# Kernel optimization log

Measured on AMD Instinct MI355X. Metric: run time of the kernel, lower is better.

The kernel has to match this reference:

```python
import jax, jax.numpy as jnp
import numpy as np

H, W = 8, 8
N = 1 + H * W          # 65 tokens (cls + patches)
DIM = 128
HEADS = 8
DH = 32
INNER = HEADS * DH     # 256
B = 64
EPS = 1e-5


def setup_inputs() -> dict:
    key = jax.random.key(0)
    ks = jax.random.split(key, 7)
    x = jax.random.normal(ks[0], (B, N, DIM), dtype=jnp.float32)
    gamma = jnp.ones((DIM,), jnp.float32)
    beta = jnp.zeros((DIM,), jnp.float32)
    # kaiming_uniform-ish init scale for linear weights
    s_qk = float(np.sqrt(1.0 / DIM))
    Wqk = jax.random.uniform(ks[1], (DIM, 2 * INNER), jnp.float32, -s_qk, s_qk)
    # per-(query, key)-position value weights: [n, n, dim, inner]
    Wv = jax.random.uniform(ks[2], (N, N, DIM, INNER), jnp.float32, -s_qk, s_qk)
    s_o = float(np.sqrt(1.0 / INNER))
    Wout = jax.random.uniform(ks[3], (INNER, DIM), jnp.float32, -s_o, s_o)
    bout = jax.random.uniform(ks[4], (DIM,), jnp.float32, -s_o, s_o)
    return {"x": x, "gamma": gamma, "beta": beta, "Wqk": Wqk, "Wv": Wv,
            "Wout": Wout, "bout": bout}


def reference(x, gamma, beta, Wqk, Wv, Wout, bout):
    b, n, d = x.shape
    # LayerNorm
    mu = jnp.mean(x, axis=-1, keepdims=True)
    var = jnp.mean(jnp.square(x - mu), axis=-1, keepdims=True)
    xn = (x - mu) / jnp.sqrt(var + EPS) * gamma + beta
    # q, k projections
    qk = xn @ Wqk                               # [b, n, 2*inner]
    q, k = jnp.split(qk, 2, axis=-1)
    q = q.reshape(b, n, HEADS, DH).transpose(0, 2, 1, 3)  # [b, h, n, dh]
    k = k.reshape(b, n, HEADS, DH).transpose(0, 2, 1, 3)
    scale = DH ** -0.5
    dots = jnp.einsum('bhnd,bhmd->bhnm', q, k) * scale
    attn = jax.nn.softmax(dots, axis=-1)        # [b, h, n, m]
    # per-(n,m) value: v[b,n,m] = xn[b,n] @ Wv[n,m]  -> [b, n, m, inner]
    v = jnp.einsum('bnd,nmde->bnme', xn, Wv)
    v = v.reshape(b, n, n, HEADS, DH)           # [b, n, m, h, dh]
    # weighted sum over keys m
    out = jnp.einsum('bhnm,bnmhd->bnhd', attn, v).reshape(b, n, INNER)
    return out @ Wout + bout
```

## Files before the change

kernel.cpp:

```cpp
#include <hip/hip_runtime.h>

#define EPS 1e-5f

typedef __attribute__((ext_vector_type(8))) short short8;
typedef __attribute__((ext_vector_type(4))) float float4v;

__device__ __forceinline__ unsigned short f2bf(float x) {
  unsigned int u = __builtin_bit_cast(unsigned int, x);
  u += 0x7fffu + ((u >> 16) & 1u);
  return (unsigned short)(u >> 16);
}
__device__ __forceinline__ float bf2f(unsigned short h) {
  unsigned int u = ((unsigned int)h) << 16;
  return __builtin_bit_cast(float, u);
}

__global__ __launch_bounds__(256) void ln_kernel(
    const float* __restrict__ x, const float* __restrict__ gamma,
    const float* __restrict__ beta, float* __restrict__ xn,
    float* __restrict__ inner) {
  {
    const int zi = blockIdx.x * 1024 + threadIdx.x * 4;
    float4 z; z.x = 0.f; z.y = 0.f; z.z = 0.f; z.w = 0.f;
    *(float4*)(inner + zi) = z;
  }
  const int row = blockIdx.x * 4 + (threadIdx.x >> 6);
  const int lane = threadIdx.x & 63;
  const float2 v = ((const float2*)(x + (size_t)row * 128))[lane];
  float s = v.x + v.y;
#pragma unroll
  for (int off = 1; off < 64; off <<= 1) s += __shfl_xor(s, off);
  const float mu = s * (1.f / 128.f);
  const float dx = v.x - mu, dy = v.y - mu;
  float qv = dx * dx + dy * dy;
#pragma unroll
  for (int off = 1; off < 64; off <<= 1) qv += __shfl_xor(qv, off);
  const float rstd = 1.f / sqrtf(qv * (1.f / 128.f) + EPS);
  const float2 g = ((const float2*)gamma)[lane];
  const float2 be = ((const float2*)beta)[lane];
  float2 o;
  o.x = dx * rstd * g.x + be.x;
  o.y = dy * rstd * g.y + be.y;
  ((float2*)(xn + (size_t)row * 128))[lane] = o;
}

__global__ __launch_bounds__(256) void qk_kernel(
    const float* __restrict__ xn, const float* __restrict__ Wqk,
    float* __restrict__ qk) {
  __shared__ float xsx[32][130];
  __shared__ float wsx[128][68];
  const int t = threadIdx.x;
  const int r0 = blockIdx.x * 32, c0 = blockIdx.y * 64;
  for (int i = t; i < 32 * 32; i += 256) {
    int r = i >> 5, c = (i & 31) << 2;
    float4 v = *(const float4*)(xn + (size_t)(r0 + r) * 128 + c);
    float* dst = &xsx[r][c];
    dst[0] = v.x; dst[1] = v.y; dst[2] = v.z; dst[3] = v.w;
  }
  for (int i = t; i < 128 * 16; i += 256) {
    int k = i >> 4, c = (i & 15) << 2;
    *(float4*)&wsx[k][c] = *(const float4*)(Wqk + (size_t)k * 512 + c0 + c);
  }
  __syncthreads();
  const int rr = (t >> 4) * 2, cc = (t & 15) * 4;
  float acc[2][4] = {{0.f, 0.f, 0.f, 0.f}, {0.f, 0.f, 0.f, 0.f}};
  for (int k = 0; k < 128; k++) {
    float4 wv4 = *(const float4*)&wsx[k][cc];
    float x0 = xsx[rr][k], x1 = xsx[rr + 1][k];
    acc[0][0] += x0 * wv4.x; acc[0][1] += x0 * wv4.y;
    acc[0][2] += x0 * wv4.z; acc[0][3] += x0 * wv4.w;
    acc[1][0] += x1 * wv4.x; acc[1][1] += x1 * wv4.y;
    acc[1][2] += x1 * wv4.z; acc[1][3] += x1 * wv4.w;
  }
#pragma unroll
  for (int r = 0; r < 2; r++) {
    float4 o;
    o.x = acc[r][0]; o.y = acc[r][1]; o.z = acc[r][2]; o.w = acc[r][3];
    *(float4*)(qk + (size_t)(r0 + rr + r) * 512 + c0 + cc) = o;
  }
}

__global__ __launch_bounds__(256) void softmax_kernel(
    const float* __restrict__ qk, float* __restrict__ attn) {
  const int b = blockIdx.x >> 3, h = blockIdx.x & 7;
  __shared__ float qs[65][33];
  __shared__ float ks[65][33];
  __shared__ float dotsS[65][66];
  __shared__ float rsum[65];
  const int t = threadIdx.x;
  for (int i = t; i < 65 * 32; i += 256) {
    int n = i >> 5, d = i & 31;
    size_t base = ((size_t)b * 65 + n) * 512 + h * 32 + d;
    qs[n][d] = qk[base];
    ks[n][d] = qk[base + 256];
  }
  __syncthreads();
  const float scale = 0.17677669529663687f;
  for (int i = t; i < 65 * 65; i += 256) {
    int n = i / 65, mm = i - n * 65;
    float s = 0.f;
#pragma unroll
    for (int d = 0; d < 32; d++) s += qs[n][d] * ks[mm][d];
    dotsS[n][mm] = s * scale;
  }
  __syncthreads();
  if (t < 65) {
    float mx = -1e30f;
    for (int mm = 0; mm < 65; mm++) mx = fmaxf(mx, dotsS[t][mm]);
    float sum = 0.f;
    for (int mm = 0; mm < 65; mm++) {
      float e = __expf(dotsS[t][mm] - mx);
      dotsS[t][mm] = e;
      sum += e;
    }
    rsum[t] = 1.f / sum;
  }
  __syncthreads();
  const size_t obase = ((size_t)b * 8 + h) * 65 * 65;
  for (int i = t; i < 65 * 65; i += 256) {
    int n = i / 65;
    attn[obase + i] = dotsS[n][i - n * 65] * rsum[n];
  }
}

__global__ __launch_bounds__(512, 2) void attnv_kernel(
    const float* __restrict__ xn, const float* __restrict__ attn,
    const float* __restrict__ Wv, float* __restrict__ inner) {
  __shared__ __align__(16) char sbuf[131072];
  __shared__ float attnL[5 * 8 * 64];
  float* xs = (float*)sbuf;
  unsigned short* wvb = (unsigned short*)sbuf;

  const int nq = blockIdx.x;
  const int mc = blockIdx.y;
  const int ms = (mc * 65) >> 4;
  const int cnt = (((mc + 1) * 65) >> 4) - ms;

  const int t = threadIdx.x;
  const int lane = t & 63;
  const int w = t >> 6;
  const int er = lane & 15, q = lane >> 4;
  const int rg = w & 1, cg = w >> 1;

  const int eS = t & 255;
  const int dS0 = (t >> 8) << 6;
  const float* wq = Wv + ((size_t)nq * 65 + ms) * 32768 + (size_t)dS0 * 256 + eS;

  float stg[64];

#define ISSUE(mm) do {                                                        \
    const float* p_ = wq + (size_t)(mm) * 32768;                              \
    _Pragma("unroll")                                                         \
    for (int i_ = 0; i_ < 64; i_++)                                           \
      stg[i_] = __builtin_nontemporal_load(p_ + (size_t)i_ * 256);            \
  } while (0)

#define CONVWRITE(buf) do {                                                   \
    unsigned short* wb_ = wvb + (size_t)(buf) * 32768 + eS * 128;             \
    const int cb_ = (t >> 8) << 3;                                            \
    _Pragma("unroll")                                                         \
    for (int jj_ = 0; jj_ < 8; jj_++) {                                       \
      short8 pk_;                                                             \
      _Pragma("unroll")                                                       \
      for (int j_ = 0; j_ < 8; j_++) pk_[j_] = (short)f2bf(stg[jj_ * 8 + j_]);\
      *(short8*)&wb_[((cb_ + jj_) ^ (eS & 15)) << 3] = pk_;                   \
    }                                                                         \
  } while (0)

  ISSUE(0);

  const int tot = cnt << 9;
  for (int i = t; i < tot; i += 512) {
    int mloc = i % cnt;
    int rest = i / cnt;
    int h = rest & 7;
    int b = rest >> 3;
    attnL[(mloc * 8 + h) * 64 + b] =
        attn[(((size_t)(b * 8 + h) * 65) + nq) * 65 + ms + mloc];
  }
  for (int i = t; i < 64 * 32; i += 512) {
    int b = i >> 5, c = (i & 31) << 2;
    float4 v = *(const float4*)(xn + ((size_t)b * 65 + nq) * 128 + c);
    float* dst = xs + b * 130 + c;
    dst[0] = v.x; dst[1] = v.y; dst[2] = v.z; dst[3] = v.w;
  }
  __syncthreads();

  short8 ah[2][4], al[2][4];
#pragma unroll
  for (int rt = 0; rt < 2; rt++) {
    const int arow = rg * 32 + rt * 16 + er;
#pragma unroll
    for (int s = 0; s < 4; s++) {
#pragma unroll
      for (int j = 0; j < 8; j++) {
        float xv = xs[arow * 130 + s * 32 + q * 8 + j];
        unsigned short hi = f2bf(xv);
        ah[rt][s][j] = (short)hi;
        al[rt][s][j] = (short)f2bf(xv - bf2f(hi));
      }
    }
  }
  __syncthreads();

  CONVWRITE(0);
  __syncthreads();

  float4v acc[2][4];
#pragma unroll
  for (int rt = 0; rt < 2; rt++)
#pragma unroll
    for (int ct = 0; ct < 4; ct++)
      acc[rt][ct] = (float4v){0.f, 0.f, 0.f, 0.f};

  for (int i = 0; i < cnt; i++) {
    if (i + 1 < cnt) ISSUE(i + 1);
    const unsigned short* wb = wvb + (size_t)(i & 1) * 32768;
    float4v P[2][4];
#pragma unroll
    for (int rt = 0; rt < 2; rt++)
#pragma unroll
      for (int ct = 0; ct < 4; ct++)
        P[rt][ct] = (float4v){0.f, 0.f, 0.f, 0.f};
    __builtin_amdgcn_s_setprio(1);
#pragma unroll
    for (int s = 0; s < 4; s++) {
      const int kc = 4 * s + q;
#pragma unroll
      for (int ct = 0; ct < 4; ct++) {
        short8 bf = *(const short8*)&wb[(cg * 64 + ct * 16 + er) * 128 + ((kc ^ er) << 3)];
        P[0][ct] = __builtin_amdgcn_mfma_f32_16x16x32_bf16(ah[0][s], bf, P[0][ct], 0, 0, 0);
        P[0][ct] = __builtin_amdgcn_mfma_f32_16x16x32_bf16(al[0][s], bf, P[0][ct], 0, 0, 0);
        P[1][ct] = __builtin_amdgcn_mfma_f32_16x16x32_bf16(ah[1][s], bf, P[1][ct], 0, 0, 0);
        P[1][ct] = __builtin_amdgcn_mfma_f32_16x16x32_bf16(al[1][s], bf, P[1][ct], 0, 0, 0);
      }
    }
    __builtin_amdgcn_s_setprio(0);
#pragma unroll
    for (int rt = 0; rt < 2; rt++) {
#pragma unroll
      for (int ct = 0; ct < 4; ct++) {
        const int h = cg * 2 + (ct >> 1);
        const float* ap = attnL + (i * 8 + h) * 64 + rg * 32 + rt * 16 + q * 4;
#pragma unroll
        for (int r = 0; r < 4; r++) acc[rt][ct][r] += ap[r] * P[rt][ct][r];
      }
    }
    if (i + 1 < cnt) CONVWRITE((i + 1) & 1);
    __syncthreads();
  }

#undef ISSUE
#undef CONVWRITE

#pragma unroll
  for (int rt = 0; rt < 2; rt++) {
#pragma unroll
    for (int ct = 0; ct < 4; ct++) {
      const int ecol = cg * 64 + ct * 16 + er;
#pragma unroll
      for (int r = 0; r < 4; r++) {
        const int b = rg * 32 + rt * 16 + q * 4 + r;
        atomicAdd(inner + ((size_t)b * 65 + nq) * 256 + ecol, acc[rt][ct][r]);
      }
    }
  }
}

__global__ __launch_bounds__(256) void outproj_kernel(
    const float* __restrict__ inner, const float* __restrict__ Wout,
    const float* __restrict__ bout, float* __restrict__ out) {
  __shared__ float isx[16][258];
  __shared__ float wsx[64][132];
  const int t = threadIdx.x;
  const int r0 = blockIdx.x * 16;
  for (int i = t; i < 16 * 64; i += 256) {
    int r = i >> 6, c = (i & 63) << 2;
    float4 v = *(const float4*)(inner + (size_t)(r0 + r) * 256 + c);
    float* dst = &isx[r][c];
    dst[0] = v.x; dst[1] = v.y; dst[2] = v.z; dst[3] = v.w;
  }
  const int rr = (t >> 5) * 2, cc = (t & 31) * 4;
  float acc[2][4] = {{0.f, 0.f, 0.f, 0.f}, {0.f, 0.f, 0.f, 0.f}};
  for (int kc = 0; kc < 4; kc++) {
    __syncthreads();
    for (int i = t; i < 64 * 32; i += 256) {
      int k = i >> 5, c = (i & 31) << 2;
      *(float4*)&wsx[k][c] = *(const float4*)(Wout + (size_t)(kc * 64 + k) * 128 + c);
    }
    __syncthreads();
#pragma unroll 8
    for (int k = 0; k < 64; k++) {
      float4 wv4 = *(const float4*)&wsx[k][cc];
      float x0 = isx[rr][kc * 64 + k];
      float x1 = isx[rr + 1][kc * 64 + k];
      acc[0][0] += x0 * wv4.x; acc[0][1] += x0 * wv4.y;
      acc[0][2] += x0 * wv4.z; acc[0][3] += x0 * wv4.w;
      acc[1][0] += x1 * wv4.x; acc[1][1] += x1 * wv4.y;
      acc[1][2] += x1 * wv4.z; acc[1][3] += x1 * wv4.w;
    }
  }
  float4 bb = *(const float4*)(bout + cc);
#pragma unroll
  for (int r = 0; r < 2; r++) {
    float4 o;
    o.x = acc[r][0] + bb.x; o.y = acc[r][1] + bb.y;
    o.z = acc[r][2] + bb.z; o.w = acc[r][3] + bb.w;
    *(float4*)(out + (size_t)(r0 + rr + r) * 128 + cc) = o;
  }
}

extern "C" void kernel_launch(void* const* d_in, const int* in_sizes, int n_in,
                              void* d_out, int out_size, void* d_ws, size_t ws_size,
                              hipStream_t stream) {
  const float* x     = (const float*)d_in[0];
  const float* gamma = (const float*)d_in[1];
  const float* beta  = (const float*)d_in[2];
  const float* Wqk   = (const float*)d_in[3];
  const float* Wv    = (const float*)d_in[4];
  const float* Wout  = (const float*)d_in[5];
  const float* bout  = (const float*)d_in[6];
  float* out = (float*)d_out;
  float* ws  = (float*)d_ws;

  float* xn    = ws;
  float* qk    = ws + 532480;
  float* attn  = ws + 2662400;
  float* inner = ws + 4825600;

  ln_kernel<<<1040, 256, 0, stream>>>(x, gamma, beta, xn, inner);
  qk_kernel<<<dim3(130, 8), 256, 0, stream>>>(xn, Wqk, qk);
  softmax_kernel<<<512, 256, 0, stream>>>(qk, attn);
  attnv_kernel<<<dim3(65, 16), 512, 0, stream>>>(xn, attn, Wv, inner);
  outproj_kernel<<<260, 256, 0, stream>>>(inner, Wout, bout, out);
}
```

Measured before the change: 806.0 us.

## Pre-convert Wv to swizzled bf16, stream it via global_load_lds, drop atomics

A new conv_kernel converts the fp32 Wv to bf16 once per call. It writes it into workspace already XOR-swizzled to match the LDS layout. attnv then copies tiles straight into LDS with global_load_lds instead of doing per-thread fp32 loads plus conversion, and the grid is reshaped: 256 threads, half the output columns per block, 8 key chunks. The atomicAdd into inner is replaced by per-chunk partial buffers that outproj sums, which also removes the zeroing in ln_kernel. The trade-off is that total DRAM traffic on Wv grows, since it is read as fp32, written as bf16 and read again, in exchange for a simpler, more latency-tolerant inner loop.

```diff
diff --git a/kernel.cpp b/kernel.cpp
--- a/kernel.cpp
+++ b/kernel.cpp
@@ -15,15 +15,39 @@
   return __builtin_bit_cast(float, u);
 }
 
+__device__ __forceinline__ void gl_lds16(const void* g, void* l) {
+  __builtin_amdgcn_global_load_lds(
+      (const __attribute__((address_space(1))) unsigned int*)g,
+      (__attribute__((address_space(3))) unsigned int*)l, 16, 0, 0);
+}
+
+__global__ __launch_bounds__(256) void conv_kernel(
+    const float* __restrict__ Wv, unsigned short* __restrict__ Wvb) {
+  const int blk = blockIdx.x;
+  const int t = threadIdx.x;
+  const float* src = Wv + (size_t)blk * 32768 + t;
+  char* dst = (char*)Wvb + (size_t)blk * 65536 + t * 256;
+  const int x = t & 15;
+#pragma unroll
+  for (int p = 0; p < 8; p++) {
+    float v[16];
+#pragma unroll
+    for (int j = 0; j < 16; j++)
+      v[j] = __builtin_nontemporal_load(src + (size_t)(p * 16 + j) * 256);
+    short8 a, b;
+#pragma unroll
+    for (int j = 0; j < 8; j++) {
+      a[j] = (short)f2bf(v[j]);
+      b[j] = (short)f2bf(v[8 + j]);
+    }
+    *(short8*)(dst + (((2 * p) ^ x) << 4)) = a;
+    *(short8*)(dst + (((2 * p + 1) ^ x) << 4)) = b;
+  }
+}
+
 __global__ __launch_bounds__(256) void ln_kernel(
     const float* __restrict__ x, const float* __restrict__ gamma,
-    const float* __restrict__ beta, float* __restrict__ xn,
-    float* __restrict__ inner) {
-  {
-    const int zi = blockIdx.x * 1024 + threadIdx.x * 4;
-    float4 z; z.x = 0.f; z.y = 0.f; z.z = 0.f; z.w = 0.f;
-    *(float4*)(inner + zi) = z;
-  }
+    const float* __restrict__ beta, float* __restrict__ xn) {
   const int row = blockIdx.x * 4 + (threadIdx.x >> 6);
   const int lane = threadIdx.x & 63;
   const float2 v = ((const float2*)(x + (size_t)row * 128))[lane];
@@ -123,69 +147,35 @@
   }
 }
 
-__global__ __launch_bounds__(512, 2) void attnv_kernel(
+__global__ __launch_bounds__(256, 2) void attnv_kernel(
     const float* __restrict__ xn, const float* __restrict__ attn,
-    const float* __restrict__ Wv, float* __restrict__ inner) {
-  __shared__ __align__(16) char sbuf[131072];
-  __shared__ float attnL[5 * 8 * 64];
+    const unsigned short* __restrict__ Wvb, float* __restrict__ inner_p) {
+  __shared__ __align__(16) char sbuf[65536];
+  __shared__ float attnL[9 * 4 * 64];
   float* xs = (float*)sbuf;
   unsigned short* wvb = (unsigned short*)sbuf;
 
-  const int nq = blockIdx.x;
+  const int nq = blockIdx.x >> 1, eh = blockIdx.x & 1;
   const int mc = blockIdx.y;
-  const int ms = (mc * 65) >> 4;
-  const int cnt = (((mc + 1) * 65) >> 4) - ms;
+  const int ms = (mc * 65) >> 3;
+  const int cnt = (((mc + 1) * 65) >> 3) - ms;
 
   const int t = threadIdx.x;
   const int lane = t & 63;
   const int w = t >> 6;
   const int er = lane & 15, q = lane >> 4;
   const int rg = w & 1, cg = w >> 1;
-
-  const int eS = t & 255;
-  const int dS0 = (t >> 8) << 6;
-  const float* wq = Wv + ((size_t)nq * 65 + ms) * 32768 + (size_t)dS0 * 256 + eS;
-
-  float stg[64];
-
-#define ISSUE(mm) do {                                                        \
-    const float* p_ = wq + (size_t)(mm) * 32768;                              \
-    _Pragma("unroll")                                                         \
-    for (int i_ = 0; i_ < 64; i_++)                                           \
-      stg[i_] = __builtin_nontemporal_load(p_ + (size_t)i_ * 256);            \
-  } while (0)
-
-#define CONVWRITE(buf) do {                                                   \
-    unsigned short* wb_ = wvb + (size_t)(buf) * 32768 + eS * 128;             \
-    const int cb_ = (t >> 8) << 3;                                            \
-    _Pragma("unroll")                                                         \
-    for (int jj_ = 0; jj_ < 8; jj_++) {                                       \
-      short8 pk_;                                                             \
-      _Pragma("unroll")                                                       \
-      for (int j_ = 0; j_ < 8; j_++) pk_[j_] = (short)f2bf(stg[jj_ * 8 + j_]);\
-      *(short8*)&wb_[((cb_ + jj_) ^ (eS & 15)) << 3] = pk_;                   \
-    }                                                                         \
-  } while (0)
-
-  ISSUE(0);
-
-  const int tot = cnt << 9;
-  for (int i = t; i < tot; i += 512) {
-    int mloc = i % cnt;
-    int rest = i / cnt;
-    int h = rest & 7;
-    int b = rest >> 3;
-    attnL[(mloc * 8 + h) * 64 + b] =
-        attn[(((size_t)(b * 8 + h) * 65) + nq) * 65 + ms + mloc];
-  }
-  for (int i = t; i < 64 * 32; i += 512) {
+  const int woff = w * 8192;
+
+  const char* wvblk = (const char*)Wvb + ((size_t)nq * 65 + ms) * 65536 + eh * 32768;
+
+  for (int i = t; i < 64 * 32; i += 256) {
     int b = i >> 5, c = (i & 31) << 2;
     float4 v = *(const float4*)(xn + ((size_t)b * 65 + nq) * 128 + c);
     float* dst = xs + b * 130 + c;
     dst[0] = v.x; dst[1] = v.y; dst[2] = v.z; dst[3] = v.w;
   }
   __syncthreads();
-
   short8 ah[2][4], al[2][4];
 #pragma unroll
   for (int rt = 0; rt < 2; rt++) {
@@ -203,7 +193,19 @@
   }
   __syncthreads();
 
-  CONVWRITE(0);
+  {
+#pragma unroll
+    for (int j = 0; j < 8; j++)
+      gl_lds16(wvblk + woff + j * 1024 + (lane << 4),
+               (char*)wvb + woff + j * 1024);
+  }
+  {
+    const int hloc = t >> 6, b = t & 63;
+    const int hg = eh * 4 + hloc;
+    for (int mloc = 0; mloc < cnt; mloc++)
+      attnL[(mloc * 4 + hloc) * 64 + b] =
+          attn[(((size_t)(b * 8 + hg)) * 65 + nq) * 65 + ms + mloc];
+  }
   __syncthreads();
 
   float4v acc[2][4];
@@ -214,8 +216,14 @@
       acc[rt][ct] = (float4v){0.f, 0.f, 0.f, 0.f};
 
   for (int i = 0; i < cnt; i++) {
-    if (i + 1 < cnt) ISSUE(i + 1);
-    const unsigned short* wb = wvb + (size_t)(i & 1) * 32768;
+    if (i + 1 < cnt) {
+      const char* gs = wvblk + (size_t)(i + 1) * 65536;
+      char* ls = (char*)wvb + ((i + 1) & 1) * 32768;
+#pragma unroll
+      for (int j = 0; j < 8; j++)
+        gl_lds16(gs + woff + j * 1024 + (lane << 4), ls + woff + j * 1024);
+    }
+    const unsigned short* wb = wvb + (i & 1) * 16384;
     float4v P[2][4];
 #pragma unroll
     for (int rt = 0; rt < 2; rt++)
@@ -240,35 +248,32 @@
     for (int rt = 0; rt < 2; rt++) {
 #pragma unroll
       for (int ct = 0; ct < 4; ct++) {
-        const int h = cg * 2 + (ct >> 1);
-        const float* ap = attnL + (i * 8 + h) * 64 + rg * 32 + rt * 16 + q * 4;
+        const int hl = cg * 2 + (ct >> 1);
+        const float* ap = attnL + (i * 4 + hl) * 64 + rg * 32 + rt * 16 + q * 4;
 #pragma unroll
         for (int r = 0; r < 4; r++) acc[rt][ct][r] += ap[r] * P[rt][ct][r];
       }
     }
-    if (i + 1 < cnt) CONVWRITE((i + 1) & 1);
     __syncthreads();
   }
 
-#undef ISSUE
-#undef CONVWRITE
-
+  float* ip = inner_p + (size_t)mc * 1064960;
 #pragma unroll
   for (int rt = 0; rt < 2; rt++) {
 #pragma unroll
     for (int ct = 0; ct < 4; ct++) {
-      const int ecol = cg * 64 + ct * 16 + er;
+      const int ecol = eh * 128 + cg * 64 + ct * 16 + er;
 #pragma unroll
       for (int r = 0; r < 4; r++) {
         const int b = rg * 32 + rt * 16 + q * 4 + r;
-        atomicAdd(inner + ((size_t)b * 65 + nq) * 256 + ecol, acc[rt][ct][r]);
+        ip[((size_t)b * 65 + nq) * 256 + ecol] = acc[rt][ct][r];
       }
     }
   }
 }
 
 __global__ __launch_bounds__(256) void outproj_kernel(
-    const float* __restrict__ inner, const float* __restrict__ Wout,
+    const float* __restrict__ inner_p, const float* __restrict__ Wout,
     const float* __restrict__ bout, float* __restrict__ out) {
   __shared__ float isx[16][258];
   __shared__ float wsx[64][132];
@@ -276,9 +281,16 @@
   const int r0 = blockIdx.x * 16;
   for (int i = t; i < 16 * 64; i += 256) {
     int r = i >> 6, c = (i & 63) << 2;
-    float4 v = *(const float4*)(inner + (size_t)(r0 + r) * 256 + c);
+    float4 a;
+    a.x = 0.f; a.y = 0.f; a.z = 0.f; a.w = 0.f;
+#pragma unroll
+    for (int jj = 0; jj < 8; jj++) {
+      float4 v = *(const float4*)(inner_p + (size_t)jj * 1064960 +
+                                  (size_t)(r0 + r) * 256 + c);
+      a.x += v.x; a.y += v.y; a.z += v.z; a.w += v.w;
+    }
     float* dst = &isx[r][c];
-    dst[0] = v.x; dst[1] = v.y; dst[2] = v.z; dst[3] = v.w;
+    dst[0] = a.x; dst[1] = a.y; dst[2] = a.z; dst[3] = a.w;
   }
   const int rr = (t >> 5) * 2, cc = (t & 31) * 4;
   float acc[2][4] = {{0.f, 0.f, 0.f, 0.f}, {0.f, 0.f, 0.f, 0.f}};
@@ -323,14 +335,16 @@
   float* out = (float*)d_out;
   float* ws  = (float*)d_ws;
 
-  float* xn    = ws;
-  float* qk    = ws + 532480;
-  float* attn  = ws + 2662400;
-  float* inner = ws + 4825600;
-
-  ln_kernel<<<1040, 256, 0, stream>>>(x, gamma, beta, xn, inner);
+  float* xn      = ws;
+  float* qk      = ws + 532480;
+  float* attn    = ws + 2662400;
+  float* inner_p = ws + 4825600;
+  unsigned short* Wvb = (unsigned short*)(ws + 13500032);
+
+  conv_kernel<<<4225, 256, 0, stream>>>(Wv, Wvb);
+  ln_kernel<<<1040, 256, 0, stream>>>(x, gamma, beta, xn);
   qk_kernel<<<dim3(130, 8), 256, 0, stream>>>(xn, Wqk, qk);
   softmax_kernel<<<512, 256, 0, stream>>>(qk, attn);
-  attnv_kernel<<<dim3(65, 16), 512, 0, stream>>>(xn, attn, Wv, inner);
-  outproj_kernel<<<260, 256, 0, stream>>>(inner, Wout, bout, out);
-}
+  attnv_kernel<<<dim3(130, 8), 256, 0, stream>>>(xn, attn, Wvb, inner_p);
+  outproj_kernel<<<260, 256, 0, stream>>>(inner_p, Wout, bout, out);
+}
```

New measurement: 980.1 us. 21.6% more time.
